# Optimization experiments

Measured on AMD Instinct MI355X. Metric: run time of the kernel, lower is better.

The kernel has to match this reference:

```python
import jax, jax.numpy as jnp
import numpy as np

LX, LY = 16, 16
N = 2 * LX * LY        # 512 lattice sites (sequence length)
NH = 128               # GRU hidden size
K = 2                  # binary occupation categories
NS = 4096              # number of Monte-Carlo samples (batch)


def setup_inputs() -> dict:
    key = jax.random.key(0)
    k0, k1, k2, k3 = jax.random.split(key, 4)
    gru_kernel = jax.random.normal(k0, (K, 3 * NH), jnp.float32) * (1.0 / np.sqrt(K))
    gru_rkernel = jax.random.normal(k1, (NH, 3 * NH), jnp.float32) * (1.0 / np.sqrt(NH))
    gru_bias = jnp.zeros((2, 3 * NH), jnp.float32)  # [input_bias; recurrent_bias] (reset_after=True)
    dense_w = jax.random.normal(k2, (NH, K), jnp.float32) * (1.0 / np.sqrt(NH))
    dense_b = jnp.zeros((K,), jnp.float32)
    u = jax.random.uniform(k3, (NS, N), jnp.float32)  # pre-drawn noise for categorical draws
    return {"gru_kernel": gru_kernel, "gru_rkernel": gru_rkernel, "gru_bias": gru_bias,
            "dense_w": dense_w, "dense_b": dense_b, "u": u}


def reference(gru_kernel, gru_rkernel, gru_bias, dense_w, dense_b, u):
    """Autoregressive GRU sampling over N lattice sites.
    Returns (samples [ns,N] int32, log_prob [ns] float32)."""
    ns = u.shape[0]
    b_in, b_rec = gru_bias[0], gru_bias[1]

    def step(carry, u_t):
        h, x = carry                       # h: [ns,NH], x: one-hot prev sample [ns,K]
        xg = x @ gru_kernel + b_in          # [ns,3NH]
        hg = h @ gru_rkernel + b_rec        # [ns,3NH]
        xz, xr, xh = jnp.split(xg, 3, axis=-1)   # keras gate order: z, r, h
        hz, hr, hh = jnp.split(hg, 3, axis=-1)
        z = jax.nn.sigmoid(xz + hz)
        r = jax.nn.sigmoid(xr + hr)
        hc = jnp.tanh(xh + r * hh)          # reset_after=True candidate
        h_new = z * h + (1.0 - z) * hc
        probs = jax.nn.softmax(h_new @ dense_w + dense_b, axis=-1)  # [ns,K]
        p1 = probs[:, 1]
        s = (u_t < p1).astype(jnp.int32)    # categorical draw (K=2) via inverse CDF
        logp_t = jnp.log(jnp.where(s == 1, p1, probs[:, 0]) + 1e-10)
        x_new = jax.nn.one_hot(s, K, dtype=h.dtype)
        return (h_new, x_new), (s, logp_t)

    h0 = jnp.zeros((ns, NH), u.dtype)
    x0 = jnp.zeros((ns, K), u.dtype)        # zero input at first site
    (_, _), (samples, logps) = jax.lax.scan(step, (h0, x0), u.T)  # scan over N sites
    return samples.T, logps.sum(axis=0)
```

## Files before the change

### kernel.cpp

```cpp
#include <hip/hip_runtime.h>

#define NHID   128
#define NSTEPS 512
#define NSAMP  4096
#define SPB    8
#define BS     256
#define NBLK   (NSAMP / SPB)
#define KL4    11
#define SAMP_ELEMS (NSAMP * NSTEPS)
#define WT_ELEMS   (3 * NHID * NHID)

typedef float v2f __attribute__((ext_vector_type(2)));
typedef float v4f __attribute__((ext_vector_type(4)));

#define PK_LO(ACC, W2, H2) \
    asm("v_pk_fma_f32 %0, %1, %2, %0 op_sel:[0,0,0] op_sel_hi:[0,1,1]" \
        : "+v"(ACC) : "v"(W2), "v"(H2))
#define PK_HI(ACC, W2, H2) \
    asm("v_pk_fma_f32 %0, %1, %2, %0 op_sel:[1,0,0] op_sel_hi:[1,1,1]" \
        : "+v"(ACC) : "v"(W2), "v"(H2))

template<int IMM>
__device__ __forceinline__ float swz(float x) {
    return __int_as_float(__builtin_amdgcn_ds_swizzle(__float_as_int(x), IMM));
}

__global__ __launch_bounds__(256)
void pack_w_kernel(const float* __restrict__ rk, float* __restrict__ wt) {
    const int i = blockIdx.x * 256 + threadIdx.x;
    if (i < WT_ELEMS) {
        const int j  = i & 3;
        const int c  = (i >> 2) & 127;
        const int k4 = (i >> 9) & 31;
        const int g  = i >> 14;
        wt[i] = rk[(k4 * 4 + j) * 384 + g * NHID + c];
    }
}

template<int TR>
__global__ __launch_bounds__(BS, 2)
void vmc_gru_kernel(const float* __restrict__ gk,
                    const float* __restrict__ rk,
                    const float* __restrict__ gb,
                    const float* __restrict__ dw,
                    const float* __restrict__ db,
                    const float* __restrict__ u,
                    const float* __restrict__ wt,
                    float* __restrict__ out)
{
    __shared__ float hsm[2][NHID][SPB];
    __shared__ float part[2][4][2][8];
    __shared__ v4f   slds[3 * KL4 * NHID];

    const int tid = threadIdx.x;
    const int cg  = tid >> 1;
    const int sq  = tid & 1;
    const int s0  = sq * 4;
    const int wv  = tid >> 6;
    const int sbase = blockIdx.x * SPB + s0;

    if (TR) {
        const v4f* wt4 = (const v4f*)wt;
        for (int i = tid; i < 3 * KL4 * NHID; i += BS) {
            const int g = i / (KL4 * NHID);
            const int r = i - g * (KL4 * NHID);
            slds[i] = wt4[g * 4096 + r];
        }
    }
    for (int i = tid; i < 2 * NHID * SPB; i += BS) (&hsm[0][0][0])[i] = 0.0f;
    __syncthreads();

    const float brz = gb[384 + cg];
    const float brr = gb[384 + 128 + cg];
    const float brh = gb[384 + 256 + cg];
    const float xzI = gb[cg],       xz0c = xzI + gk[cg],       xz1c = xzI + gk[384 + cg];
    const float xrI = gb[128 + cg], xr0c = xrI + gk[128 + cg], xr1c = xrI + gk[384 + 128 + cg];
    const float xhI = gb[256 + cg], xh0c = xhI + gk[256 + cg], xh1c = xhI + gk[384 + 256 + cg];
    const float dwc0 = dw[cg * 2], dwc1 = dw[cg * 2 + 1];
    const float db0 = db[0], db1 = db[1];

    const v4f* lz = slds + cg;
    const v4f* lr = slds + KL4 * 128 + cg;
    const v4f* lh = slds + 2 * KL4 * 128 + cg;
    const v4f* wz4 = (const v4f*)wt + cg;
    const v4f* wr4 = (const v4f*)wt + 4096 + cg;
    const v4f* wh4 = (const v4f*)wt + 8192 + cg;
    const float* rkp = rk + cg;

    int   pv[4] = {0, 0, 0, 0};
    float lg[4] = {0.f, 0.f, 0.f, 0.f};
    float pr[4] = {1.f, 1.f, 1.f, 1.f};
    int cur = 0;

    for (int t = 0; t < NSTEPS; ++t) {
        float uv[4];
        #pragma unroll
        for (int j = 0; j < 4; ++j)
            uv[j] = u[(size_t)(sbase + j) * NSTEPS + t];

        v2f az01 = {brz, brz}, az23 = {brz, brz};
        v2f ar01 = {brr, brr}, ar23 = {brr, brr};
        v2f ah01 = {brh, brh}, ah23 = {brh, brh};
        const float* hb = &hsm[cur][0][0];

#define GEMM_K4(WZ, WR, WH, K4) do {                                      \
    const v4f h0 = *(const v4f*)(hb + (4*(K4)+0)*SPB + s0);               \
    const v4f h1 = *(const v4f*)(hb + (4*(K4)+1)*SPB + s0);               \
    const v4f h2 = *(const v4f*)(hb + (4*(K4)+2)*SPB + s0);               \
    const v4f h3 = *(const v4f*)(hb + (4*(K4)+3)*SPB + s0);               \
    const v2f wzA = (WZ).xy, wzB = (WZ).zw;                               \
    const v2f wrA = (WR).xy, wrB = (WR).zw;                               \
    const v2f whA = (WH).xy, whB = (WH).zw;                               \
    PK_LO(az01, wzA, h0.xy); PK_LO(az23, wzA, h0.zw);                     \
    PK_LO(ar01, wrA, h0.xy); PK_LO(ar23, wrA, h0.zw);                     \
    PK_LO(ah01, whA, h0.xy); PK_LO(ah23, whA, h0.zw);                     \
    PK_HI(az01, wzA, h1.xy); PK_HI(az23, wzA, h1.zw);                     \
    PK_HI(ar01, wrA, h1.xy); PK_HI(ar23, wrA, h1.zw);                     \
    PK_HI(ah01, whA, h1.xy); PK_HI(ah23, whA, h1.zw);                     \
    PK_LO(az01, wzB, h2.xy); PK_LO(az23, wzB, h2.zw);                     \
    PK_LO(ar01, wrB, h2.xy); PK_LO(ar23, wrB, h2.zw);                     \
    PK_LO(ah01, whB, h2.xy); PK_LO(ah23, whB, h2.zw);                     \
    PK_HI(az01, wzB, h3.xy); PK_HI(az23, wzB, h3.zw);                     \
    PK_HI(ar01, wrB, h3.xy); PK_HI(ar23, wrB, h3.zw);                     \
    PK_HI(ah01, whB, h3.xy); PK_HI(ah23, whB, h3.zw);                     \
} while (0)

        if (TR) {
            #pragma unroll 4
            for (int k4 = 0; k4 < KL4; ++k4) {
                const v4f wz = lz[k4 * 128];
                const v4f wr = lr[k4 * 128];
                const v4f wh = lh[k4 * 128];
                GEMM_K4(wz, wr, wh, k4);
            }
            #pragma unroll 4
            for (int k4 = KL4; k4 < 32; ++k4) {
                const v4f wz = wz4[k4 * 128];
                const v4f wr = wr4[k4 * 128];
                const v4f wh = wh4[k4 * 128];
                GEMM_K4(wz, wr, wh, k4);
            }
        } else {
            const float* wp = rkp;
            #pragma unroll 4
            for (int k = 0; k < NHID; ++k) {
                const float wzs = wp[0];
                const float wrs = wp[NHID];
                const float whs = wp[2 * NHID];
                const v4f hv = *(const v4f*)(hb + k * SPB + s0);
                const float hk[4] = {hv.x, hv.y, hv.z, hv.w};
                float azs[4] = {az01.x, az01.y, az23.x, az23.y};
                float ars[4] = {ar01.x, ar01.y, ar23.x, ar23.y};
                float ahs[4] = {ah01.x, ah01.y, ah23.x, ah23.y};
                #pragma unroll
                for (int j = 0; j < 4; ++j) azs[j] = fmaf(wzs, hk[j], azs[j]);
                #pragma unroll
                for (int j = 0; j < 4; ++j) ars[j] = fmaf(wrs, hk[j], ars[j]);
                #pragma unroll
                for (int j = 0; j < 4; ++j) ahs[j] = fmaf(whs, hk[j], ahs[j]);
                az01 = (v2f){azs[0], azs[1]}; az23 = (v2f){azs[2], azs[3]};
                ar01 = (v2f){ars[0], ars[1]}; ar23 = (v2f){ars[2], ars[3]};
                ah01 = (v2f){ahs[0], ahs[1]}; ah23 = (v2f){ahs[2], ahs[3]};
                wp += 3 * NHID;
            }
        }
#undef GEMM_K4

        const float az[4] = {az01.x, az01.y, az23.x, az23.y};
        const float ar[4] = {ar01.x, ar01.y, ar23.x, ar23.y};
        const float ah[4] = {ah01.x, ah01.y, ah23.x, ah23.y};

        const v4f ho = *(const v4f*)(hb + cg * SPB + s0);
        const float hov[4] = {ho.x, ho.y, ho.z, ho.w};
        float hn[4], p0s[4], p1s[4];
        #pragma unroll
        for (int j = 0; j < 4; ++j) {
            float xz = pv[j] ? xz1c : xz0c;
            float xr = pv[j] ? xr1c : xr0c;
            float xh = pv[j] ? xh1c : xh0c;
            if (t == 0) { xz = xzI; xr = xrI; xh = xhI; }
            const float z  = 1.0f / (1.0f + expf(-(xz + az[j])));
            const float r  = 1.0f / (1.0f + expf(-(xr + ar[j])));
            const float hc = tanhf(xh + r * ah[j]);
            const float hnew = z * hov[j] + (1.0f - z) * hc;
            hn[j] = hnew;
            p0s[j] = hnew * dwc0;
            p1s[j] = hnew * dwc1;
        }
        *(v4f*)&hsm[cur ^ 1][cg][s0] = (v4f){hn[0], hn[1], hn[2], hn[3]};

        #pragma unroll
        for (int j = 0; j < 4; ++j) {
            p0s[j] += swz<0x081F>(p0s[j]);  p1s[j] += swz<0x081F>(p1s[j]);
            p0s[j] += swz<0x101F>(p0s[j]);  p1s[j] += swz<0x101F>(p1s[j]);
            p0s[j] += swz<0x201F>(p0s[j]);  p1s[j] += swz<0x201F>(p1s[j]);
            p0s[j] += swz<0x401F>(p0s[j]);  p1s[j] += swz<0x401F>(p1s[j]);
            p0s[j] += __shfl_xor(p0s[j], 32);
            p1s[j] += __shfl_xor(p1s[j], 32);
        }
        const int pb = t & 1;
        if ((tid & 63) < 2) {
            *(float4*)&part[pb][wv][sq][0] = make_float4(p0s[0], p0s[1], p0s[2], p0s[3]);
            *(float4*)&part[pb][wv][sq][4] = make_float4(p1s[0], p1s[1], p1s[2], p1s[3]);
        }
        __syncthreads();

        float l0[4] = {db0, db0, db0, db0};
        float l1[4] = {db1, db1, db1, db1};
        #pragma unroll
        for (int w = 0; w < 4; ++w) {
            const float4 a = *(const float4*)&part[pb][w][sq][0];
            const float4 b = *(const float4*)&part[pb][w][sq][4];
            l0[0] += a.x; l0[1] += a.y; l0[2] += a.z; l0[3] += a.w;
            l1[0] += b.x; l1[1] += b.y; l1[2] += b.z; l1[3] += b.w;
        }
        #pragma unroll
        for (int j = 0; j < 4; ++j) {
            const float mx = fmaxf(l0[j], l1[j]);
            const float e0 = expf(l0[j] - mx);
            const float e1 = expf(l1[j] - mx);
            const float inv = 1.0f / (e0 + e1);
            const float p1v = e1 * inv;
            const int st = (uv[j] < p1v) ? 1 : 0;
            const float psel = st ? p1v : (e0 * inv);
            pr[j] *= (psel + 1e-10f);
            pv[j] = st;
            if (cg == 0)
                out[(size_t)(sbase + j) * NSTEPS + t] = (float)st;
        }
        if ((t & 7) == 7) {
            #pragma unroll
            for (int j = 0; j < 4; ++j) { lg[j] += logf(pr[j]); pr[j] = 1.0f; }
        }
        cur ^= 1;
    }

    if (cg == 0) {
        #pragma unroll
        for (int j = 0; j < 4; ++j)
            out[SAMP_ELEMS + sbase + j] = lg[j];
    }
}

extern "C" void kernel_launch(void* const* d_in, const int* in_sizes, int n_in,
                              void* d_out, int out_size, void* d_ws, size_t ws_size,
                              hipStream_t stream) {
    const float* gk = (const float*)d_in[0];
    const float* rk = (const float*)d_in[1];
    const float* gb = (const float*)d_in[2];
    const float* dw = (const float*)d_in[3];
    const float* db = (const float*)d_in[4];
    const float* u  = (const float*)d_in[5];
    float* out = (float*)d_out;

    if (ws_size >= (size_t)WT_ELEMS * sizeof(float)) {
        float* wt = (float*)d_ws;
        pack_w_kernel<<<(WT_ELEMS + 255) / 256, 256, 0, stream>>>(rk, wt);
        vmc_gru_kernel<1><<<NBLK, BS, 0, stream>>>(gk, rk, gb, dw, db, u, wt, out);
    } else {
        vmc_gru_kernel<0><<<NBLK, BS, 0, stream>>>(gk, rk, gb, dw, db, u, rk, out);
    }
}
```

Baseline: 4.040 ms.

## Process 16 samples per block with two hidden columns per thread

Doubles samples per block to 16 and has each thread compute two hidden columns (c and c+64) over 4 samples. Each weight fetch is then reused across twice as many samples, halving the number of blocks and the total weight traffic. The LDS-resident share of weights grows from 11 to 20 k4 slices. Occupancy drops to one block per CU and per-thread register pressure roughly doubles, which may limit latency hiding. There are only 256 blocks, which may underfill the GPU.

```diff
diff --git a/kernel.cpp b/kernel.cpp
--- a/kernel.cpp
+++ b/kernel.cpp
@@ -3,10 +3,10 @@
 #define NHID   128
 #define NSTEPS 512
 #define NSAMP  4096
-#define SPB    8
+#define SPB    16
 #define BS     256
 #define NBLK   (NSAMP / SPB)
-#define KL4    11
+#define KL     20
 #define SAMP_ELEMS (NSAMP * NSTEPS)
 #define WT_ELEMS   (3 * NHID * NHID)
 
@@ -37,8 +37,26 @@
     }
 }
 
+#define GEMM_CH(WZ, WR, WH, AZ01, AZ23, AR01, AR23, AH01, AH23) do {      \
+    const v2f wzA = (WZ).xy, wzB = (WZ).zw;                               \
+    const v2f wrA = (WR).xy, wrB = (WR).zw;                               \
+    const v2f whA = (WH).xy, whB = (WH).zw;                               \
+    PK_LO(AZ01, wzA, h0.xy); PK_LO(AZ23, wzA, h0.zw);                     \
+    PK_LO(AR01, wrA, h0.xy); PK_LO(AR23, wrA, h0.zw);                     \
+    PK_LO(AH01, whA, h0.xy); PK_LO(AH23, whA, h0.zw);                     \
+    PK_HI(AZ01, wzA, h1.xy); PK_HI(AZ23, wzA, h1.zw);                     \
+    PK_HI(AR01, wrA, h1.xy); PK_HI(AR23, wrA, h1.zw);                     \
+    PK_HI(AH01, whA, h1.xy); PK_HI(AH23, whA, h1.zw);                     \
+    PK_LO(AZ01, wzB, h2.xy); PK_LO(AZ23, wzB, h2.zw);                     \
+    PK_LO(AR01, wrB, h2.xy); PK_LO(AR23, wrB, h2.zw);                     \
+    PK_LO(AH01, whB, h2.xy); PK_LO(AH23, whB, h2.zw);                     \
+    PK_HI(AZ01, wzB, h3.xy); PK_HI(AZ23, wzB, h3.zw);                     \
+    PK_HI(AR01, wrB, h3.xy); PK_HI(AR23, wrB, h3.zw);                     \
+    PK_HI(AH01, whB, h3.xy); PK_HI(AH23, whB, h3.zw);                     \
+} while (0)
+
 template<int TR>
-__global__ __launch_bounds__(BS, 2)
+__global__ __launch_bounds__(BS, 1)
 void vmc_gru_kernel(const float* __restrict__ gk,
                     const float* __restrict__ rk,
                     const float* __restrict__ gb,
@@ -48,44 +66,48 @@
                     const float* __restrict__ wt,
                     float* __restrict__ out)
 {
+    __shared__ v4f   slds[3 * KL * NHID];
     __shared__ float hsm[2][NHID][SPB];
-    __shared__ float part[2][4][2][8];
-    __shared__ v4f   slds[3 * KL4 * NHID];
+    __shared__ float part[2][4][SPB][2];
 
     const int tid = threadIdx.x;
-    const int cg  = tid >> 1;
-    const int sq  = tid & 1;
+    const int cg  = tid >> 2;
+    const int sq  = tid & 3;
     const int s0  = sq * 4;
     const int wv  = tid >> 6;
     const int sbase = blockIdx.x * SPB + s0;
 
     if (TR) {
         const v4f* wt4 = (const v4f*)wt;
-        for (int i = tid; i < 3 * KL4 * NHID; i += BS) {
-            const int g = i / (KL4 * NHID);
-            const int r = i - g * (KL4 * NHID);
+        for (int i = tid; i < 3 * KL * NHID; i += BS) {
+            const int g = i / (KL * NHID);
+            const int r = i - g * (KL * NHID);
             slds[i] = wt4[g * 4096 + r];
         }
     }
     for (int i = tid; i < 2 * NHID * SPB; i += BS) (&hsm[0][0][0])[i] = 0.0f;
     __syncthreads();
 
-    const float brz = gb[384 + cg];
-    const float brr = gb[384 + 128 + cg];
-    const float brh = gb[384 + 256 + cg];
-    const float xzI = gb[cg],       xz0c = xzI + gk[cg],       xz1c = xzI + gk[384 + cg];
-    const float xrI = gb[128 + cg], xr0c = xrI + gk[128 + cg], xr1c = xrI + gk[384 + 128 + cg];
-    const float xhI = gb[256 + cg], xh0c = xhI + gk[256 + cg], xh1c = xhI + gk[384 + 256 + cg];
-    const float dwc0 = dw[cg * 2], dwc1 = dw[cg * 2 + 1];
+    const int c0 = cg, c1 = cg + 64;
+    const float brzA = gb[384 + c0],       brzB = gb[384 + c1];
+    const float brrA = gb[384 + 128 + c0], brrB = gb[384 + 128 + c1];
+    const float brhA = gb[384 + 256 + c0], brhB = gb[384 + 256 + c1];
+    const float xzIA = gb[c0],       xz0A = xzIA + gk[c0],       xz1A = xzIA + gk[384 + c0];
+    const float xrIA = gb[128 + c0], xr0A = xrIA + gk[128 + c0], xr1A = xrIA + gk[384 + 128 + c0];
+    const float xhIA = gb[256 + c0], xh0A = xhIA + gk[256 + c0], xh1A = xhIA + gk[384 + 256 + c0];
+    const float xzIB = gb[c1],       xz0B = xzIB + gk[c1],       xz1B = xzIB + gk[384 + c1];
+    const float xrIB = gb[128 + c1], xr0B = xrIB + gk[128 + c1], xr1B = xrIB + gk[384 + 128 + c1];
+    const float xhIB = gb[256 + c1], xh0B = xhIB + gk[256 + c1], xh1B = xhIB + gk[384 + 256 + c1];
+    const float dw0A = dw[c0 * 2], dw1A = dw[c0 * 2 + 1];
+    const float dw0B = dw[c1 * 2], dw1B = dw[c1 * 2 + 1];
     const float db0 = db[0], db1 = db[1];
 
-    const v4f* lz = slds + cg;
-    const v4f* lr = slds + KL4 * 128 + cg;
-    const v4f* lh = slds + 2 * KL4 * 128 + cg;
-    const v4f* wz4 = (const v4f*)wt + cg;
-    const v4f* wr4 = (const v4f*)wt + 4096 + cg;
-    const v4f* wh4 = (const v4f*)wt + 8192 + cg;
-    const float* rkp = rk + cg;
+    const v4f* lzA = slds + c0;
+    const v4f* lrA = slds + KL * 128 + c0;
+    const v4f* lhA = slds + 2 * KL * 128 + c0;
+    const v4f* gzA = (const v4f*)wt + c0;
+    const v4f* grA = (const v4f*)wt + 4096 + c0;
+    const v4f* ghA = (const v4f*)wt + 8192 + c0;
 
     int   pv[4] = {0, 0, 0, 0};
     float lg[4] = {0.f, 0.f, 0.f, 0.f};
@@ -98,100 +120,108 @@
         for (int j = 0; j < 4; ++j)
             uv[j] = u[(size_t)(sbase + j) * NSTEPS + t];
 
-        v2f az01 = {brz, brz}, az23 = {brz, brz};
-        v2f ar01 = {brr, brr}, ar23 = {brr, brr};
-        v2f ah01 = {brh, brh}, ah23 = {brh, brh};
+        v2f az01a = {brzA, brzA}, az23a = {brzA, brzA};
+        v2f ar01a = {brrA, brrA}, ar23a = {brrA, brrA};
+        v2f ah01a = {brhA, brhA}, ah23a = {brhA, brhA};
+        v2f az01b = {brzB, brzB}, az23b = {brzB, brzB};
+        v2f ar01b = {brrB, brrB}, ar23b = {brrB, brrB};
+        v2f ah01b = {brhB, brhB}, ah23b = {brhB, brhB};
         const float* hb = &hsm[cur][0][0];
-
-#define GEMM_K4(WZ, WR, WH, K4) do {                                      \
-    const v4f h0 = *(const v4f*)(hb + (4*(K4)+0)*SPB + s0);               \
-    const v4f h1 = *(const v4f*)(hb + (4*(K4)+1)*SPB + s0);               \
-    const v4f h2 = *(const v4f*)(hb + (4*(K4)+2)*SPB + s0);               \
-    const v4f h3 = *(const v4f*)(hb + (4*(K4)+3)*SPB + s0);               \
-    const v2f wzA = (WZ).xy, wzB = (WZ).zw;                               \
-    const v2f wrA = (WR).xy, wrB = (WR).zw;                               \
-    const v2f whA = (WH).xy, whB = (WH).zw;                               \
-    PK_LO(az01, wzA, h0.xy); PK_LO(az23, wzA, h0.zw);                     \
-    PK_LO(ar01, wrA, h0.xy); PK_LO(ar23, wrA, h0.zw);                     \
-    PK_LO(ah01, whA, h0.xy); PK_LO(ah23, whA, h0.zw);                     \
-    PK_HI(az01, wzA, h1.xy); PK_HI(az23, wzA, h1.zw);                     \
-    PK_HI(ar01, wrA, h1.xy); PK_HI(ar23, wrA, h1.zw);                     \
-    PK_HI(ah01, whA, h1.xy); PK_HI(ah23, whA, h1.zw);                     \
-    PK_LO(az01, wzB, h2.xy); PK_LO(az23, wzB, h2.zw);                     \
-    PK_LO(ar01, wrB, h2.xy); PK_LO(ar23, wrB, h2.zw);                     \
-    PK_LO(ah01, whB, h2.xy); PK_LO(ah23, whB, h2.zw);                     \
-    PK_HI(az01, wzB, h3.xy); PK_HI(az23, wzB, h3.zw);                     \
-    PK_HI(ar01, wrB, h3.xy); PK_HI(ar23, wrB, h3.zw);                     \
-    PK_HI(ah01, whB, h3.xy); PK_HI(ah23, whB, h3.zw);                     \
-} while (0)
 
         if (TR) {
             #pragma unroll 4
-            for (int k4 = 0; k4 < KL4; ++k4) {
-                const v4f wz = lz[k4 * 128];
-                const v4f wr = lr[k4 * 128];
-                const v4f wh = lh[k4 * 128];
-                GEMM_K4(wz, wr, wh, k4);
+            for (int k4 = 0; k4 < KL; ++k4) {
+                const v4f h0 = *(const v4f*)(hb + (4*k4+0)*SPB + s0);
+                const v4f h1 = *(const v4f*)(hb + (4*k4+1)*SPB + s0);
+                const v4f h2 = *(const v4f*)(hb + (4*k4+2)*SPB + s0);
+                const v4f h3 = *(const v4f*)(hb + (4*k4+3)*SPB + s0);
+                const v4f wza = lzA[k4*128],      wzb = lzA[k4*128 + 64];
+                const v4f wra = lrA[k4*128],      wrb = lrA[k4*128 + 64];
+                const v4f wha = lhA[k4*128],      whb = lhA[k4*128 + 64];
+                GEMM_CH(wza, wra, wha, az01a, az23a, ar01a, ar23a, ah01a, ah23a);
+                GEMM_CH(wzb, wrb, whb, az01b, az23b, ar01b, ar23b, ah01b, ah23b);
             }
             #pragma unroll 4
-            for (int k4 = KL4; k4 < 32; ++k4) {
-                const v4f wz = wz4[k4 * 128];
-                const v4f wr = wr4[k4 * 128];
-                const v4f wh = wh4[k4 * 128];
-                GEMM_K4(wz, wr, wh, k4);
+            for (int k4 = KL; k4 < 32; ++k4) {
+                const v4f h0 = *(const v4f*)(hb + (4*k4+0)*SPB + s0);
+                const v4f h1 = *(const v4f*)(hb + (4*k4+1)*SPB + s0);
+                const v4f h2 = *(const v4f*)(hb + (4*k4+2)*SPB + s0);
+                const v4f h3 = *(const v4f*)(hb + (4*k4+3)*SPB + s0);
+                const v4f wza = gzA[k4*128],      wzb = gzA[k4*128 + 64];
+                const v4f wra = grA[k4*128],      wrb = grA[k4*128 + 64];
+                const v4f wha = ghA[k4*128],      whb = ghA[k4*128 + 64];
+                GEMM_CH(wza, wra, wha, az01a, az23a, ar01a, ar23a, ah01a, ah23a);
+                GEMM_CH(wzb, wrb, whb, az01b, az23b, ar01b, ar23b, ah01b, ah23b);
             }
         } else {
-            const float* wp = rkp;
+            const float* wp = rk;
             #pragma unroll 4
             for (int k = 0; k < NHID; ++k) {
-                const float wzs = wp[0];
-                const float wrs = wp[NHID];
-                const float whs = wp[2 * NHID];
                 const v4f hv = *(const v4f*)(hb + k * SPB + s0);
                 const float hk[4] = {hv.x, hv.y, hv.z, hv.w};
-                float azs[4] = {az01.x, az01.y, az23.x, az23.y};
-                float ars[4] = {ar01.x, ar01.y, ar23.x, ar23.y};
-                float ahs[4] = {ah01.x, ah01.y, ah23.x, ah23.y};
+                const float wzsA = wp[c0],       wzsB = wp[c1];
+                const float wrsA = wp[128 + c0], wrsB = wp[128 + c1];
+                const float whsA = wp[256 + c0], whsB = wp[256 + c1];
+                float aza[4] = {az01a.x, az01a.y, az23a.x, az23a.y};
+                float ara[4] = {ar01a.x, ar01a.y, ar23a.x, ar23a.y};
+                float aha[4] = {ah01a.x, ah01a.y, ah23a.x, ah23a.y};
+                float azb[4] = {az01b.x, az01b.y, az23b.x, az23b.y};
+                float arb[4] = {ar01b.x, ar01b.y, ar23b.x, ar23b.y};
+                float ahb[4] = {ah01b.x, ah01b.y, ah23b.x, ah23b.y};
                 #pragma unroll
-                for (int j = 0; j < 4; ++j) azs[j] = fmaf(wzs, hk[j], azs[j]);
-                #pragma unroll
-                for (int j = 0; j < 4; ++j) ars[j] = fmaf(wrs, hk[j], ars[j]);
-                #pragma unroll
-                for (int j = 0; j < 4; ++j) ahs[j] = fmaf(whs, hk[j], ahs[j]);
-                az01 = (v2f){azs[0], azs[1]}; az23 = (v2f){azs[2], azs[3]};
-                ar01 = (v2f){ars[0], ars[1]}; ar23 = (v2f){ars[2], ars[3]};
-                ah01 = (v2f){ahs[0], ahs[1]}; ah23 = (v2f){ahs[2], ahs[3]};
-                wp += 3 * NHID;
+                for (int j = 0; j < 4; ++j) {
+                    aza[j] = fmaf(wzsA, hk[j], aza[j]); ara[j] = fmaf(wrsA, hk[j], ara[j]);
+                    aha[j] = fmaf(whsA, hk[j], aha[j]);
+                    azb[j] = fmaf(wzsB, hk[j], azb[j]); arb[j] = fmaf(wrsB, hk[j], arb[j]);
+                    ahb[j] = fmaf(whsB, hk[j], ahb[j]);
+                }
+                az01a = (v2f){aza[0], aza[1]}; az23a = (v2f){aza[2], aza[3]};
+                ar01a = (v2f){ara[0], ara[1]}; ar23a = (v2f){ara[2], ara[3]};
+                ah01a = (v2f){aha[0], aha[1]}; ah23a = (v2f){aha[2], aha[3]};
+                az01b = (v2f){azb[0], azb[1]}; az23b = (v2f){azb[2], azb[3]};
+                ar01b = (v2f){arb[0], arb[1]}; ar23b = (v2f){arb[2], arb[3]};
+                ah01b = (v2f){ahb[0], ahb[1]}; ah23b = (v2f){ahb[2], ahb[3]};
+                wp += 384;
             }
         }
-#undef GEMM_K4
-
-        const float az[4] = {az01.x, az01.y, az23.x, az23.y};
-        const float ar[4] = {ar01.x, ar01.y, ar23.x, ar23.y};
-        const float ah[4] = {ah01.x, ah01.y, ah23.x, ah23.y};
-
-        const v4f ho = *(const v4f*)(hb + cg * SPB + s0);
-        const float hov[4] = {ho.x, ho.y, ho.z, ho.w};
-        float hn[4], p0s[4], p1s[4];
+
+        const float azA[4] = {az01a.x, az01a.y, az23a.x, az23a.y};
+        const float arA[4] = {ar01a.x, ar01a.y, ar23a.x, ar23a.y};
+        const float ahA[4] = {ah01a.x, ah01a.y, ah23a.x, ah23a.y};
+        const float azB[4] = {az01b.x, az01b.y, az23b.x, az23b.y};
+        const float arB[4] = {ar01b.x, ar01b.y, ar23b.x, ar23b.y};
+        const float ahB[4] = {ah01b.x, ah01b.y, ah23b.x, ah23b.y};
+
+        const v4f hoA = *(const v4f*)(hb + c0 * SPB + s0);
+        const v4f hoB = *(const v4f*)(hb + c1 * SPB + s0);
+        const float hovA[4] = {hoA.x, hoA.y, hoA.z, hoA.w};
+        const float hovB[4] = {hoB.x, hoB.y, hoB.z, hoB.w};
+        float hnA[4], hnB[4], p0s[4], p1s[4];
         #pragma unroll
         for (int j = 0; j < 4; ++j) {
-            float xz = pv[j] ? xz1c : xz0c;
-            float xr = pv[j] ? xr1c : xr0c;
-            float xh = pv[j] ? xh1c : xh0c;
-            if (t == 0) { xz = xzI; xr = xrI; xh = xhI; }
-            const float z  = 1.0f / (1.0f + expf(-(xz + az[j])));
-            const float r  = 1.0f / (1.0f + expf(-(xr + ar[j])));
-            const float hc = tanhf(xh + r * ah[j]);
-            const float hnew = z * hov[j] + (1.0f - z) * hc;
-            hn[j] = hnew;
-            p0s[j] = hnew * dwc0;
-            p1s[j] = hnew * dwc1;
-        }
-        *(v4f*)&hsm[cur ^ 1][cg][s0] = (v4f){hn[0], hn[1], hn[2], hn[3]};
+            float xzA = pv[j] ? xz1A : xz0A, xzB = pv[j] ? xz1B : xz0B;
+            float xrA = pv[j] ? xr1A : xr0A, xrB = pv[j] ? xr1B : xr0B;
+            float xhA = pv[j] ? xh1A : xh0A, xhB = pv[j] ? xh1B : xh0B;
+            if (t == 0) { xzA = xzIA; xrA = xrIA; xhA = xhIA;
+                          xzB = xzIB; xrB = xrIB; xhB = xhIB; }
+            const float zA  = 1.0f / (1.0f + expf(-(xzA + azA[j])));
+            const float rA  = 1.0f / (1.0f + expf(-(xrA + arA[j])));
+            const float hcA = tanhf(xhA + rA * ahA[j]);
+            const float hA2 = zA * hovA[j] + (1.0f - zA) * hcA;
+            const float zB  = 1.0f / (1.0f + expf(-(xzB + azB[j])));
+            const float rB  = 1.0f / (1.0f + expf(-(xrB + arB[j])));
+            const float hcB = tanhf(xhB + rB * ahB[j]);
+            const float hB2 = zB * hovB[j] + (1.0f - zB) * hcB;
+            hnA[j] = hA2;
+            hnB[j] = hB2;
+            p0s[j] = fmaf(hB2, dw0B, hA2 * dw0A);
+            p1s[j] = fmaf(hB2, dw1B, hA2 * dw1A);
+        }
+        *(v4f*)&hsm[cur ^ 1][c0][s0] = (v4f){hnA[0], hnA[1], hnA[2], hnA[3]};
+        *(v4f*)&hsm[cur ^ 1][c1][s0] = (v4f){hnB[0], hnB[1], hnB[2], hnB[3]};
 
         #pragma unroll
         for (int j = 0; j < 4; ++j) {
-            p0s[j] += swz<0x081F>(p0s[j]);  p1s[j] += swz<0x081F>(p1s[j]);
             p0s[j] += swz<0x101F>(p0s[j]);  p1s[j] += swz<0x101F>(p1s[j]);
             p0s[j] += swz<0x201F>(p0s[j]);  p1s[j] += swz<0x201F>(p1s[j]);
             p0s[j] += swz<0x401F>(p0s[j]);  p1s[j] += swz<0x401F>(p1s[j]);
@@ -199,9 +229,9 @@
             p1s[j] += __shfl_xor(p1s[j], 32);
         }
         const int pb = t & 1;
-        if ((tid & 63) < 2) {
-            *(float4*)&part[pb][wv][sq][0] = make_float4(p0s[0], p0s[1], p0s[2], p0s[3]);
-            *(float4*)&part[pb][wv][sq][4] = make_float4(p1s[0], p1s[1], p1s[2], p1s[3]);
+        if ((tid & 63) < 4) {
+            *(float4*)&part[pb][wv][s0][0]     = make_float4(p0s[0], p1s[0], p0s[1], p1s[1]);
+            *(float4*)&part[pb][wv][s0 + 2][0] = make_float4(p0s[2], p1s[2], p0s[3], p1s[3]);
         }
         __syncthreads();
 
@@ -209,10 +239,12 @@
         float l1[4] = {db1, db1, db1, db1};
         #pragma unroll
         for (int w = 0; w < 4; ++w) {
-            const float4 a = *(const float4*)&part[pb][w][sq][0];
-            const float4 b = *(const float4*)&part[pb][w][sq][4];
-            l0[0] += a.x; l0[1] += a.y; l0[2] += a.z; l0[3] += a.w;
-            l1[0] += b.x; l1[1] += b.y; l1[2] += b.z; l1[3] += b.w;
+            const float4 qa = *(const float4*)&part[pb][w][s0][0];
+            const float4 qb = *(const float4*)&part[pb][w][s0 + 2][0];
+            l0[0] += qa.x; l1[0] += qa.y;
+            l0[1] += qa.z; l1[1] += qa.w;
+            l0[2] += qb.x; l1[2] += qb.y;
+            l0[3] += qb.z; l1[3] += qb.w;
         }
         #pragma unroll
         for (int j = 0; j < 4; ++j) {
```

New measurement: 4.714 ms. 16.7% more time.
